# Kernel optimization log

Measured on AMD Instinct MI355X. Metric: run time of the kernel, lower is better.

## Reference

```python
import jax, jax.numpy as jnp
import numpy as np

H, D, K, FF = 4, 256, 1024, 1024  # n_head, d_model, key_feature_dim, dim_feedforward
L, B = 2048, 4                    # pixels, batch


def setup_inputs() -> dict:
    key = jax.random.key(0)
    ks = jax.random.split(key, 12)
    def g(k, shape, s=0.02):
        return jax.random.normal(k, shape, jnp.float32) * s
    return dict(
        src=jax.random.normal(ks[0], (L, B, D), jnp.float32),
        WK=g(ks[1], (H, K, D), (2.0 / K) ** 0.5),
        WQ=g(ks[2], (H, K, D), (2.0 / K) ** 0.5),
        WV=g(ks[3], (H, D, D), (2.0 / D) ** 0.5),
        TC=g(ks[4], (H, D, D)),
        ENw1=g(ks[5], (H, FF, D)), ENb1=jnp.zeros((H, FF), jnp.float32),
        ENw2=g(ks[6], (H, D, FF)), ENb2=jnp.zeros((H, D), jnp.float32),
        ENg=jnp.ones((H, D), jnp.float32), ENbeta=jnp.zeros((H, D), jnp.float32),
        Wout=g(ks[7], (D, H * D)),
        L1w=g(ks[8], (FF, D)), L1b=jnp.zeros((FF,), jnp.float32),
        L2w=g(ks[9], (D, FF)), L2b=jnp.zeros((D,), jnp.float32),
        N1g=jnp.ones((D,), jnp.float32), N1b=jnp.zeros((D,), jnp.float32),
        N2g=jnp.ones((D,), jnp.float32), N2b=jnp.zeros((D,), jnp.float32),
    )


def _ln(x, g, b, eps=1e-5):
    m = jnp.mean(x, -1, keepdims=True)
    v = jnp.mean((x - m) ** 2, -1, keepdims=True)
    return (x - m) * jax.lax.rsqrt(v + eps) * g + b


def _l2n(x, eps=1e-12):
    n = jnp.sqrt(jnp.sum(x * x, -1, keepdims=True))
    return x / jnp.maximum(n, eps)


def reference(src, WK, WQ, WV, TC, ENw1, ENb1, ENw2, ENb2, ENg, ENbeta,
              Wout, L1w, L1b, L2w, L2b, N1g, N1b, N2g, N2b):
    # --- RMA: per-head RelationUnit, vectorized over head axis h ---
    wq = _l2n(jnp.einsum('lbd,hkd->hlbk', src, WQ))   # (H,L,B,K), L2-normed
    wk = _l2n(jnp.einsum('lbd,hkd->hlbk', src, WK))
    wv = jnp.einsum('lbd,hed->hlbe', src, WV)         # (H,L,B,D)
    dot = jnp.einsum('hlbk,hmbk->hblm', wq, wk)       # (H,B,Lq,Lk)
    aff = jax.nn.softmax(dot, axis=-1)                 # softmax over keys (temp=1)
    aff = aff / (1e-9 + jnp.sum(aff, axis=2, keepdims=True))  # renorm over QUERY dim (torch dim=1)
    out = jnp.einsum('hblm,hmbe->hlbe', aff, wv)       # (H,L,B,D)
    ru = jax.nn.relu(jnp.einsum('hlbe,hfe->hlbf', src[None] - out, TC))
    # per-head extra TransNonlinear: residual MLP + layernorm
    hid = jax.nn.relu(jnp.einsum('hlbd,hfd->hlbf', ru, ENw1) + ENb1[:, None, None, :])
    s2 = jnp.einsum('hlbf,hdf->hlbd', hid, ENw2) + ENb2[:, None, None, :]
    tn = _ln(ru + s2, ENg[:, None, None, :], ENbeta[:, None, None, :])  # (H,L,B,D)
    concat = jnp.transpose(tn, (1, 2, 0, 3)).reshape(L, B, H * D)
    attn = concat @ Wout.T                              # (L,B,D)
    # --- encoder layer: residual + LN + FFN + LN (dropout = eval identity) ---
    x = _ln(src + attn, N1g, N1b)
    ff = jax.nn.relu(x @ L1w.T + L1b) @ L2w.T + L2b
    return _ln(x + ff, N2g, N2b)
```

## Files before the change

### kernel.cpp

```cpp
#include <hip/hip_runtime.h>
#include <hip/hip_bf16.h>

typedef __hip_bfloat16 bf16;
typedef short s16x8 __attribute__((ext_vector_type(8)));
typedef float f32x4 __attribute__((ext_vector_type(4)));

#define HN 4
#define DM 256
#define KF 1024
#define FFD 1024
#define LL 2048
#define BB 4
#define NN (LL * BB)
#define HD (HN * DM)

__device__ __forceinline__ float b2f(unsigned short u) {
    unsigned v = ((unsigned)u) << 16; float f; __builtin_memcpy(&f, &v, 4); return f;
}
__device__ __forceinline__ unsigned short f2b(float f) {
    bf16 b = (bf16)f; unsigned short u; __builtin_memcpy(&u, &b, 2); return u;
}

__device__ __forceinline__ float waveReduceSum(float v) {
    for (int o = 32; o; o >>= 1) v += __shfl_down(v, o, 64);
    return v;
}
__device__ __forceinline__ float waveReduceMax(float v) {
    for (int o = 32; o; o >>= 1) v = fmaxf(v, __shfl_down(v, o, 64));
    return v;
}
__device__ __forceinline__ float blockReduceSum(float v) {
    __shared__ float sh[4];
    v = waveReduceSum(v);
    __syncthreads();
    if ((threadIdx.x & 63) == 0) sh[threadIdx.x >> 6] = v;
    __syncthreads();
    return sh[0] + sh[1] + sh[2] + sh[3];
}
__device__ __forceinline__ float blockReduceMax(float v) {
    __shared__ float sh[4];
    v = waveReduceMax(v);
    __syncthreads();
    if ((threadIdx.x & 63) == 0) sh[threadIdx.x >> 6] = v;
    __syncthreads();
    return fmaxf(fmaxf(sh[0], sh[1]), fmaxf(sh[2], sh[3]));
}

__global__ void sentinel_kernel(float* out, float val) {
    if (threadIdx.x == 0 && blockIdx.x == 0) out[0] = val;
}

__device__ __forceinline__ void gll16(const void* g, void* l) {
#if defined(__HIP_DEVICE_COMPILE__)
    __builtin_amdgcn_global_load_lds(
        (const __attribute__((address_space(1))) unsigned int*)g,
        (__attribute__((address_space(3))) unsigned int*)l, 16, 0, 0);
#endif
}

#define VMC(n) asm volatile("s_waitcnt vmcnt(" #n ")" ::: "memory")
#define LGKM0() asm volatile("s_waitcnt lgkmcnt(0)" ::: "memory")

__global__ __launch_bounds__(512) void gemm256(
    const bf16* __restrict__ A, int lda, long sA,
    const bf16* __restrict__ Bv, int ldb, long sB,
    void* __restrict__ C, int cF32, int ldc, long sC,
    int Kc,
    const float* __restrict__ bias, long sBias,
    const void* __restrict__ aux, int auxType, int ldaux, long sAux,
    float accSign, int relu)
{
    const int z = blockIdx.z;
    const bf16* Ah = A + (long)z * sA;
    const bf16* Bh = Bv + (long)z * sB;
    float* Cf = (float*)C + (long)z * sC;
    bf16*  Ch = (bf16*)C + (long)z * sC;
    const float* biasp = bias ? (bias + (long)z * sBias) : nullptr;
    const float* auxf = (auxType == 1) ? ((const float*)aux + (long)z * sAux) : nullptr;
    const bf16*  auxh = (auxType == 2) ? ((const bf16*)aux + (long)z * sAux) : nullptr;

    __shared__ __align__(16) bf16 As[2][256 * 64];
    __shared__ __align__(16) bf16 Bs[2][256 * 64];

    const int tid  = threadIdx.x;
    const int lane = tid & 63;
    const int wid  = __builtin_amdgcn_readfirstlane(tid >> 6);
    const int wm   = wid >> 2;
    const int wn   = wid & 3;
    const int lrow = lane & 15;
    const int quad = lane >> 4;
    const int m0 = blockIdx.x * 256;
    const int n0 = blockIdx.y * 256;

    const int srow8  = wid * 8 + (lane >> 3);
    const int scolsw = ((lane & 7) * 8) ^ ((srow8 & 7) << 3);
    const bf16* Aorg = Ah + (long)m0 * lda;
    const bf16* Borg = Bh + (long)n0 * ldb;

    const int colx = (lane & 7) << 3;
    const int kc0 = (quad * 8) ^ colx;
    const int kc1 = (32 + quad * 8) ^ colx;

    f32x4 acc[8][4] = {};
    s16x8 afr[4][2], bfr[4][2];

    const int nk = Kc >> 6;

    auto stg = [&](const bf16* org, int ld, bf16* lds, int k0, int h) {
#pragma unroll
        for (int j = 0; j < 2; j++) {
            int rl = h * 128 + j * 64 + srow8;
            gll16((const void*)(org + (long)rl * ld + k0 + scolsw),
                  (void*)(lds + (h * 128 + j * 64 + wid * 8) * 64));
        }
    };

    stg(Aorg, lda, As[0], 0, 0); stg(Aorg, lda, As[0], 0, 1);
    stg(Borg, ldb, Bs[0], 0, 0); stg(Borg, ldb, Bs[0], 0, 1);
    if (nk > 1) {
        stg(Aorg, lda, As[1], 64, 0); stg(Aorg, lda, As[1], 64, 1);
        stg(Borg, ldb, Bs[1], 64, 0); stg(Borg, ldb, Bs[1], 64, 1);
        VMC(8);
    } else {
        VMC(0);
    }
    __builtin_amdgcn_s_barrier();

    for (int t = 0; t < nk; ++t) {
        const int s = t & 1;
        const bf16* Acur = As[s];
        const bf16* Bcur = Bs[s];
        bf16* Anxt = As[s ^ 1];
        bf16* Bslot = Bs[s];
        const bool stA = (t >= 1) && (t + 1 < nk);
        const bool stB = (t + 2 < nk);

#pragma unroll
        for (int mi = 0; mi < 4; mi++) {
            int r = (wm * 128 + mi * 16 + lrow) * 64;
            afr[mi][0] = *(const s16x8*)&Acur[r + kc0];
            afr[mi][1] = *(const s16x8*)&Acur[r + kc1];
        }
#pragma unroll
        for (int ni = 0; ni < 2; ni++) {
            int r = (wn * 64 + ni * 16 + lrow) * 64;
            bfr[ni][0] = *(const s16x8*)&Bcur[r + kc0];
            bfr[ni][1] = *(const s16x8*)&Bcur[r + kc1];
        }
        if (stA) stg(Aorg, lda, Anxt, (t + 1) << 6, 0);
        __builtin_amdgcn_s_barrier();
        LGKM0();
        __builtin_amdgcn_s_setprio(1);
#pragma unroll
        for (int mi = 0; mi < 4; mi++)
#pragma unroll
            for (int ni = 0; ni < 2; ni++)
#pragma unroll
                for (int ks = 0; ks < 2; ks++)
                    acc[mi][ni] = __builtin_amdgcn_mfma_f32_16x16x32_bf16(afr[mi][ks], bfr[ni][ks], acc[mi][ni], 0, 0, 0);
        __builtin_amdgcn_s_setprio(0);
        __builtin_amdgcn_s_barrier();

#pragma unroll
        for (int ni = 0; ni < 2; ni++) {
            int r = (wn * 64 + (2 + ni) * 16 + lrow) * 64;
            bfr[2 + ni][0] = *(const s16x8*)&Bcur[r + kc0];
            bfr[2 + ni][1] = *(const s16x8*)&Bcur[r + kc1];
        }
        if (stA) stg(Aorg, lda, Anxt, (t + 1) << 6, 1);
        __builtin_amdgcn_s_barrier();
        LGKM0();
        __builtin_amdgcn_s_setprio(1);
#pragma unroll
        for (int mi = 0; mi < 4; mi++)
#pragma unroll
            for (int ni = 0; ni < 2; ni++)
#pragma unroll
                for (int ks = 0; ks < 2; ks++)
                    acc[mi][2 + ni] = __builtin_amdgcn_mfma_f32_16x16x32_bf16(afr[mi][ks], bfr[2 + ni][ks], acc[mi][2 + ni], 0, 0, 0);
        __builtin_amdgcn_s_setprio(0);
        __builtin_amdgcn_s_barrier();

#pragma unroll
        for (int mi = 0; mi < 4; mi++) {
            int r = (wm * 128 + 64 + mi * 16 + lrow) * 64;
            afr[mi][0] = *(const s16x8*)&Acur[r + kc0];
            afr[mi][1] = *(const s16x8*)&Acur[r + kc1];
        }
        if (stB) stg(Borg, ldb, Bslot, (t + 2) << 6, 0);
        __builtin_amdgcn_s_barrier();
        LGKM0();
        __builtin_amdgcn_s_setprio(1);
#pragma unroll
        for (int mi = 0; mi < 4; mi++)
#pragma unroll
            for (int ni = 0; ni < 2; ni++)
#pragma unroll
                for (int ks = 0; ks < 2; ks++)
                    acc[4 + mi][ni] = __builtin_amdgcn_mfma_f32_16x16x32_bf16(afr[mi][ks], bfr[ni][ks], acc[4 + mi][ni], 0, 0, 0);
        __builtin_amdgcn_s_setprio(0);
        __builtin_amdgcn_s_barrier();

        if (stB) stg(Borg, ldb, Bslot, (t + 2) << 6, 1);
        __builtin_amdgcn_s_barrier();
        __builtin_amdgcn_s_setprio(1);
#pragma unroll
        for (int mi = 0; mi < 4; mi++)
#pragma unroll
            for (int ni = 0; ni < 2; ni++)
#pragma unroll
                for (int ks = 0; ks < 2; ks++)
                    acc[4 + mi][2 + ni] = __builtin_amdgcn_mfma_f32_16x16x32_bf16(afr[mi][ks], bfr[2 + ni][ks], acc[4 + mi][2 + ni], 0, 0, 0);
        __builtin_amdgcn_s_setprio(0);
        if (stB) { VMC(4); } else { VMC(0); }
        __builtin_amdgcn_s_barrier();
    }

#pragma unroll
    for (int mi = 0; mi < 8; mi++) {
#pragma unroll
        for (int ni = 0; ni < 4; ni++) {
            int col = n0 + wn * 64 + ni * 16 + lrow;
            float bvl = biasp ? biasp[col] : 0.0f;
#pragma unroll
            for (int i = 0; i < 4; i++) {
                int row = m0 + wm * 128 + mi * 16 + quad * 4 + i;
                float v = accSign * acc[mi][ni][i] + bvl;
                if (auxType == 1) v += auxf[(long)row * ldaux + col];
                else if (auxType == 2) v += (float)auxh[(long)row * ldaux + col];
                if (relu) v = fmaxf(v, 0.0f);
                if (cF32) Cf[(long)row * ldc + col] = v;
                else Ch[(long)row * ldc + col] = (bf16)v;
            }
        }
    }
}

template<int BN>
__global__ __launch_bounds__(256) void gemm_nt(
    const void* __restrict__ A, int aF32, int lda, long sA,
    const void* __restrict__ Bv, int bF32, int ldb, long sB,
    void* __restrict__ C, int cF32, int ldc, long sC,
    int Kc,
    const float* __restrict__ bias, long sBias,
    const void* __restrict__ aux, int auxType, int ldaux, long sAux,
    float accSign, int relu)
{
    constexpr int NI = BN / 32;
    constexpr int WN = BN / 2;
    const int z = blockIdx.z;
    const float* Af = (const float*)A + (long)z * sA;
    const bf16*  Ah = (const bf16*)A + (long)z * sA;
    const float* Bf = (const float*)Bv + (long)z * sB;
    const bf16*  Bh = (const bf16*)Bv + (long)z * sB;
    float* Cf = (float*)C + (long)z * sC;
    bf16*  Ch = (bf16*)C + (long)z * sC;
    const float* biasp = bias ? (bias + (long)z * sBias) : nullptr;
    const float* auxf = (auxType == 1) ? ((const float*)aux + (long)z * sAux) : nullptr;
    const bf16*  auxh = (auxType == 2) ? ((const bf16*)aux + (long)z * sAux) : nullptr;

    __shared__ __align__(16) bf16 As[3][128 * 32];
    __shared__ __align__(16) bf16 Bs[3][BN * 32];

    const int tid = threadIdx.x;
    const int lane = tid & 63;
    const int wv = __builtin_amdgcn_readfirstlane(tid >> 6);
    const int wm = (tid >> 6) & 1;
    const int wn = (tid >> 6) >> 1;
    const int lrow = lane & 15;
    const int quad = lane >> 4;
    const int m0 = blockIdx.x * 128;
    const int n0 = blockIdx.y * BN;
    const int srow = tid >> 1;
    const int scol = (tid & 1) * 16;
    const int drow = wv * 16 + (lane >> 2);
    const int dcol = (lane & 3) * 8;

    f32x4 acc[4][NI] = {};

    if (!aF32 && !bF32) {
        const int nk = Kc >> 5;
        auto stage = [&](int t) {
            const int buf = t % 3;
            const int k0 = t << 5;
            const bf16* a0 = Ah + (long)(m0 + drow) * lda + k0 + dcol;
            gll16((const void*)a0, (void*)&As[buf][wv * 512]);
            gll16((const void*)(a0 + (long)lda * 64), (void*)&As[buf][2048 + wv * 512]);
            const bf16* b0 = Bh + (long)(n0 + drow) * ldb + k0 + dcol;
            gll16((const void*)b0, (void*)&Bs[buf][wv * 512]);
            if (BN == 128)
                gll16((const void*)(b0 + (long)ldb * 64), (void*)&Bs[buf][2048 + wv * 512]);
        };
        stage(0);
        if (nk > 1) {
            stage(1);
            if constexpr (BN == 128) { VMC(4); } else { VMC(3); }
        } else {
            VMC(0);
        }
        __builtin_amdgcn_s_barrier();
        for (int t = 0; t < nk; ++t) {
            const int cur = t % 3;
            if (t + 2 < nk) stage(t + 2);
            s16x8 af[4], bfg[NI];
#pragma unroll
            for (int mi = 0; mi < 4; mi++)
                af[mi] = *(const s16x8*)&As[cur][(wm * 64 + mi * 16 + lrow) * 32 + quad * 8];
#pragma unroll
            for (int ni = 0; ni < NI; ni++)
                bfg[ni] = *(const s16x8*)&Bs[cur][(wn * WN + ni * 16 + lrow) * 32 + quad * 8];
#pragma unroll
            for (int mi = 0; mi < 4; mi++)
#pragma unroll
                for (int ni = 0; ni < NI; ni++)
                    acc[mi][ni] = __builtin_amdgcn_mfma_f32_16x16x32_bf16(af[mi], bfg[ni], acc[mi][ni], 0, 0, 0);
            if (t + 2 < nk) {
                if constexpr (BN == 128) { VMC(4); } else { VMC(3); }
            } else {
                VMC(0);
            }
            __builtin_amdgcn_s_barrier();
        }
    } else {
        for (int k0 = 0; k0 < Kc; k0 += 32) {
            uint4 av0, av1, bv0, bv1;
            if (aF32) {
                const float* ag = Af + (long)(m0 + srow) * lda + k0 + scol;
                ushort t[16];
#pragma unroll
                for (int j = 0; j < 4; j++) {
                    float4 f = *(const float4*)(ag + 4 * j);
                    t[4*j] = f2b(f.x); t[4*j+1] = f2b(f.y); t[4*j+2] = f2b(f.z); t[4*j+3] = f2b(f.w);
                }
                av0 = *(const uint4*)&t[0]; av1 = *(const uint4*)&t[8];
            }
            if (bF32) {
                if (srow < BN) {
                    const float* bg = Bf + (long)(n0 + srow) * ldb + k0 + scol;
                    ushort t[16];
#pragma unroll
                    for (int j = 0; j < 4; j++) {
                        float4 f = *(const float4*)(bg + 4 * j);
                        t[4*j] = f2b(f.x); t[4*j+1] = f2b(f.y); t[4*j+2] = f2b(f.z); t[4*j+3] = f2b(f.w);
                    }
                    bv0 = *(const uint4*)&t[0]; bv1 = *(const uint4*)&t[8];
                }
            }
            __syncthreads();
            if (aF32) {
                *(uint4*)&As[0][srow * 32 + scol] = av0;
                *(uint4*)&As[0][srow * 32 + scol + 8] = av1;
            } else {
                gll16((const void*)(Ah + (long)(m0 + drow) * lda + k0 + dcol), (void*)&As[0][wv * 512]);
                gll16((const void*)(Ah + (long)(m0 + 64 + drow) * lda + k0 + dcol), (void*)&As[0][2048 + wv * 512]);
            }
            if (bF32) {
                if (srow < BN) {
                    *(uint4*)&Bs[0][srow * 32 + scol] = bv0;
                    *(uint4*)&Bs[0][srow * 32 + scol + 8] = bv1;
                }
            } else {
                gll16((const void*)(Bh + (long)(n0 + drow) * ldb + k0 + dcol), (void*)&Bs[0][wv * 512]);
                if (BN == 128)
                    gll16((const void*)(Bh + (long)(n0 + 64 + drow) * ldb + k0 + dcol), (void*)&Bs[0][2048 + wv * 512]);
            }
            __syncthreads();

            s16x8 af[4], bfg[NI];
#pragma unroll
            for (int mi = 0; mi < 4; mi++)
                af[mi] = *(const s16x8*)&As[0][(wm * 64 + mi * 16 + lrow) * 32 + quad * 8];
#pragma unroll
            for (int ni = 0; ni < NI; ni++)
                bfg[ni] = *(const s16x8*)&Bs[0][(wn * WN + ni * 16 + lrow) * 32 + quad * 8];
#pragma unroll
            for (int mi = 0; mi < 4; mi++)
#pragma unroll
                for (int ni = 0; ni < NI; ni++)
                    acc[mi][ni] = __builtin_amdgcn_mfma_f32_16x16x32_bf16(af[mi], bfg[ni], acc[mi][ni], 0, 0, 0);
        }
    }

#pragma unroll
    for (int mi = 0; mi < 4; mi++) {
#pragma unroll
        for (int ni = 0; ni < NI; ni++) {
            int col = n0 + wn * WN + ni * 16 + lrow;
            float bvl = biasp ? biasp[col] : 0.0f;
#pragma unroll
            for (int i = 0; i < 4; i++) {
                int row = m0 + wm * 64 + mi * 16 + quad * 4 + i;
                float v = accSign * acc[mi][ni][i] + bvl;
                if (auxType == 1) v += auxf[(long)row * ldaux + col];
                else if (auxType == 2) v += (float)auxh[(long)row * ldaux + col];
                if (relu) v = fmaxf(v, 0.0f);
                if (cF32) Cf[(long)row * ldc + col] = v;
                else Ch[(long)row * ldc + col] = (bf16)v;
            }
        }
    }
}

__global__ __launch_bounds__(256) void cvt4(const float* __restrict__ in, bf16* __restrict__ out, int n4) {
    int i = blockIdx.x * 256 + threadIdx.x;
    if (i < n4) {
        float4 f = ((const float4*)in)[i];
        ushort4 u; u.x = f2b(f.x); u.y = f2b(f.y); u.z = f2b(f.z); u.w = f2b(f.w);
        ((ushort4*)out)[i] = u;
    }
}

struct WCvt {
    const float* in[16];
    bf16* out[16];
    int n4[16];
};
__global__ __launch_bounds__(256) void cvt_weights(WCvt wc) {
    int t = blockIdx.y;
    int n4 = wc.n4[t];
    const float4* in = (const float4*)wc.in[t];
    ushort4* out = (ushort4*)wc.out[t];
    for (int i = blockIdx.x * 256 + threadIdx.x; i < n4; i += gridDim.x * 256) {
        float4 f = in[i];
        ushort4 u; u.x = f2b(f.x); u.y = f2b(f.y); u.z = f2b(f.z); u.w = f2b(f.w);
        out[i] = u;
    }
}

__global__ __launch_bounds__(256) void l2norm_rows(bf16* __restrict__ Q) {
    bf16* q = Q + (long)blockIdx.x * KF;
    ushort4 u = ((ushort4*)q)[threadIdx.x];
    float v0 = b2f(u.x), v1 = b2f(u.y), v2 = b2f(u.z), v3 = b2f(u.w);
    float ss = blockReduceSum(v0 * v0 + v1 * v1 + v2 * v2 + v3 * v3);
    float inv = 1.0f / fmaxf(sqrtf(ss), 1e-12f);
    u.x = f2b(v0 * inv); u.y = f2b(v1 * inv); u.z = f2b(v2 * inv); u.w = f2b(v3 * inv);
    ((ushort4*)q)[threadIdx.x] = u;
}

__global__ __launch_bounds__(256) void l2norm2(bf16* __restrict__ QK) {
    bf16* q = QK + (long)blockIdx.x * 2048 + (long)blockIdx.y * 1024;
    ushort4 u = ((ushort4*)q)[threadIdx.x];
    float v0 = b2f(u.x), v1 = b2f(u.y), v2 = b2f(u.z), v3 = b2f(u.w);
    float ss = blockReduceSum(v0 * v0 + v1 * v1 + v2 * v2 + v3 * v3);
    float inv = 1.0f / fmaxf(sqrtf(ss), 1e-12f);
    u.x = f2b(v0 * inv); u.y = f2b(v1 * inv); u.z = f2b(v2 * inv); u.w = f2b(v3 * inv);
    ((ushort4*)q)[threadIdx.x] = u;
}

__global__ __launch_bounds__(256) void softmax_rows(bf16* __restrict__ P) {
    bf16* p = P + (long)blockIdx.x * LL;
    ushort4 a = ((ushort4*)p)[2 * threadIdx.x];
    ushort4 b = ((ushort4*)p)[2 * threadIdx.x + 1];
    float v[8] = {b2f(a.x), b2f(a.y), b2f(a.z), b2f(a.w), b2f(b.x), b2f(b.y), b2f(b.z), b2f(b.w)};
    float mx = -1e30f;
#pragma unroll
    for (int i = 0; i < 8; i++) mx = fmaxf(mx, v[i]);
    mx = blockReduceMax(mx);
    float s = 0.0f;
#pragma unroll
    for (int i = 0; i < 8; i++) { v[i] = __expf(v[i] - mx); s += v[i]; }
    s = blockReduceSum(s);
    float inv = 1.0f / s;
    a.x = f2b(v[0]*inv); a.y = f2b(v[1]*inv); a.z = f2b(v[2]*inv); a.w = f2b(v[3]*inv);
    b.x = f2b(v[4]*inv); b.y = f2b(v[5]*inv); b.z = f2b(v[6]*inv); b.w = f2b(v[7]*inv);
    ((ushort4*)p)[2 * threadIdx.x] = a;
    ((ushort4*)p)[2 * threadIdx.x + 1] = b;
}

__global__ __launch_bounds__(256) void zero_cs(float* __restrict__ cs) {
    cs[blockIdx.x * 256 + threadIdx.x] = 0.0f;
}

__global__ __launch_bounds__(256) void colsum2(const bf16* __restrict__ P, float* __restrict__ cs) {
    int col = blockIdx.x * 256 + threadIdx.x;
    int rc = blockIdx.y;
    int b = blockIdx.z;
    const bf16* p = P + (long)b * LL * LL + (long)rc * 128 * LL + col;
    float s = 0.0f;
#pragma unroll 4
    for (int r = 0; r < 128; r++) s += (float)p[(long)r * LL];
    atomicAdd(&cs[(long)b * LL + col], s);
}

__global__ __launch_bounds__(256) void scale_vt(bf16* __restrict__ vt, const float* __restrict__ cs) {
    int e = blockIdx.x, b = blockIdx.y;
    bf16* row = vt + ((long)b * DM + e) * LL;
    const float* c = cs + (long)b * LL;
#pragma unroll
    for (int i = 0; i < 8; i++) {
        int m = threadIdx.x + i * 256;
        row[m] = (bf16)((float)row[m] / (1e-9f + c[m]));
    }
}

__global__ __launch_bounds__(256) void ln_rows(const bf16* __restrict__ in, void* __restrict__ out,
                                               int outF32,
                                               const float* __restrict__ g, const float* __restrict__ b,
                                               const float* __restrict__ aux) {
    long base = (long)blockIdx.x * 256;
    float v = (float)in[base + threadIdx.x];
    if (aux) v += aux[base + threadIdx.x];
    float mean = blockReduceSum(v) * (1.0f / 256.0f);
    float d = v - mean;
    float var = blockReduceSum(d * d) * (1.0f / 256.0f);
    float o = d * rsqrtf(var + 1e-5f) * g[threadIdx.x] + b[threadIdx.x];
    if (outF32) ((float*)out)[base + threadIdx.x] = o;
    else ((bf16*)out)[base + threadIdx.x] = (bf16)o;
}

__global__ __launch_bounds__(256) void ln_cat(bf16* __restrict__ cat, const float* __restrict__ g,
                                              const float* __restrict__ bb) {
    long n = blockIdx.x;
    int h = blockIdx.y;
    bf16* x = cat + n * HD + (long)h * DM;
    float v = (float)x[threadIdx.x];
    float mean = blockReduceSum(v) * (1.0f / 256.0f);
    float d = v - mean;
    float var = blockReduceSum(d * d) * (1.0f / 256.0f);
    x[threadIdx.x] = (bf16)(d * rsqrtf(var + 1e-5f) * g[h * DM + threadIdx.x] + bb[h * DM + threadIdx.x]);
}

extern "C" void kernel_launch(void* const* d_in, const int* in_sizes, int n_in,
                              void* d_out, int out_size, void* d_ws, size_t ws_size,
                              hipStream_t stream) {
    const float* src  = (const float*)d_in[0];
    const float* WK   = (const float*)d_in[1];
    const float* WQ   = (const float*)d_in[2];
    const float* WV   = (const float*)d_in[3];
    const float* TC   = (const float*)d_in[4];
    const float* ENw1 = (const float*)d_in[5];
    const float* ENb1 = (const float*)d_in[6];
    const float* ENw2 = (const float*)d_in[7];
    const float* ENb2 = (const float*)d_in[8];
    const float* ENg  = (const float*)d_in[9];
    const float* ENbt = (const float*)d_in[10];
    const float* Wout = (const float*)d_in[11];
    const float* L1w  = (const float*)d_in[12];
    const float* L1b  = (const float*)d_in[13];
    const float* L2w  = (const float*)d_in[14];
    const float* L2b  = (const float*)d_in[15];
    const float* N1g  = (const float*)d_in[16];
    const float* N1b  = (const float*)d_in[17];
    const float* N2g  = (const float*)d_in[18];
    const float* N2b  = (const float*)d_in[19];

    const size_t COMPACT_FLOOR = 34700000;
    const size_t FAST_FLOOR  = 92307456;
    const size_t FASTW_FLOOR = 92307456 + 11010048;
    if (ws_size < COMPACT_FLOOR || out_size != NN * DM || n_in != 20) {
        float val;
        if (n_in != 20) val = 32768.0f + (float)n_in;
        else if (out_size != NN * DM) val = 49152.0f;
        else val = 16384.0f + 128.0f * (float)(unsigned)(ws_size >> 20);
        sentinel_kernel<<<1, 64, 0, stream>>>((float*)d_out, val);
        return;
    }

    char* w = (char*)d_ws;
    auto G = [&](const void* A, int aF, int lda, long sA,
                 const void* B, int bF, int ldb, long sB,
                 void* C, int cF, int ldc, long sC,
                 int M, int Nn, int Kc, int nb,
                 const float* bias, long sBias,
                 const void* aux, int auxT, int ldaux, long sAux,
                 float sgn, int relu) {
        gemm_nt<128><<<dim3(M / 128, Nn / 128, nb), dim3(256), 0, stream>>>(
            A, aF, lda, sA, B, bF, ldb, sB, C, cF, ldc, sC, Kc,
            bias, sBias, aux, auxT, ldaux, sAux, sgn, relu);
    };
    auto G64 = [&](const void* A, int aF, int lda, long sA,
                 const void* B, int bF, int ldb, long sB,
                 void* C, int cF, int ldc, long sC,
                 int M, int Nn, int Kc, int nb,
                 const float* bias, long sBias,
                 const void* aux, int auxT, int ldaux, long sAux,
                 float sgn, int relu) {
        gemm_nt<64><<<dim3(M / 128, Nn / 64, nb), dim3(256), 0, stream>>>(
            A, aF, lda, sA, B, bF, ldb, sB, C, cF, ldc, sC, Kc,
            bias, sBias, aux, auxT, ldaux, sAux, sgn, relu);
    };
    auto G2 = [&](const void* A, int lda, long sA,
                  const void* B, int ldb, long sB,
                  void* C, int cF, int ldc, long sC,
                  int M, int Nn, int Kc, int nb,
                  const float* bias, long sBias,
                  const void* aux, int auxT, int ldaux, long sAux,
                  float sgn, int relu) {
        gemm256<<<dim3(M / 256, Nn / 256, nb), dim3(512), 0, stream>>>(
            (const bf16*)A, lda, sA, (const bf16*)B, ldb, sB, C, cF, ldc, sC, Kc,
            bias, sBias, aux, auxT, ldaux, sAux, sgn, relu);
    };

    if (ws_size >= FAST_FLOOR) {
        bf16*  Sb  = (bf16*)(w + 0);
        bf16*  Q   = (bf16*)(w + 4194304);
        bf16*  K   = (bf16*)(w + 20971520);
        bf16*  Vt  = (bf16*)(w + 37748736);
        bf16*  P   = (bf16*)(w + 41943040);
        bf16*  Su  = (bf16*)(w + 75497472);
        float* Cs  = (float*)(w + 92274688);
        bf16* QK = Q;
        bf16* Ru = Q; bf16* Hid = K; bf16* Cat = P;
        bf16* Attn = Vt; bf16* Xln = Su; bf16* Ffh = Q; bf16* Yp = Vt;

        const int haveWb = (ws_size >= FASTW_FLOOR) ? 1 : 0;
        char* wb = w + 92307456;
        bf16* WQKb  = (bf16*)(wb + 0);
        bf16* WVb   = (bf16*)(wb + 4194304);
        bf16* TCb   = (bf16*)(wb + 4718592);
        bf16* ENw1b = (bf16*)(wb + 5242880);
        bf16* ENw2b = (bf16*)(wb + 7340032);
        bf16* Woutb = (bf16*)(wb + 9437184);
        bf16* L1wb  = (bf16*)(wb + 9961472);
        bf16* L2wb  = (bf16*)(wb + 10485760);
        if (haveWb) {
            WCvt wc;
            for (int h = 0; h < HN; h++) {
                wc.in[2*h]   = WQ + (long)h * KF * DM; wc.out[2*h]   = WQKb + (long)h * 2048 * DM;            wc.n4[2*h]   = 65536;
                wc.in[2*h+1] = WK + (long)h * KF * DM; wc.out[2*h+1] = WQKb + (long)h * 2048 * DM + KF * DM;  wc.n4[2*h+1] = 65536;
            }
            wc.in[8]  = WV;   wc.out[8]  = WVb;   wc.n4[8]  = 65536;
            wc.in[9]  = TC;   wc.out[9]  = TCb;   wc.n4[9]  = 65536;
            wc.in[10] = ENw1; wc.out[10] = ENw1b; wc.n4[10] = 262144;
            wc.in[11] = ENw2; wc.out[11] = ENw2b; wc.n4[11] = 262144;
            wc.in[12] = Wout; wc.out[12] = Woutb; wc.n4[12] = 65536;
            wc.in[13] = L1w;  wc.out[13] = L1wb;  wc.n4[13] = 65536;
            wc.in[14] = L2w;  wc.out[14] = L2wb;  wc.n4[14] = 65536;
            cvt_weights<<<dim3(256, 15), 256, 0, stream>>>(wc);
        }
        const int wF = haveWb ? 0 : 1;
        auto WP = [&](const void* f32p, const void* b16p, long off) {
            return haveWb ? (const void*)((const bf16*)b16p + off)
                          : (const void*)((const float*)f32p + off);
        };

        cvt4<<<2048, 256, 0, stream>>>(src, Sb, NN * DM / 4);

        for (int h = 0; h < HN; h++) {
            if (haveWb) {
                G2(Sb, DM, 0, WQKb + (long)h * 2048 * DM, DM, 0, QK, 0, 2048, 0,
                   NN, 2048, DM, 1, nullptr, 0, nullptr, 0, 0, 0, 1.0f, 0);
            } else {
                G(Sb, 0, DM, 0, WQ + (long)h * KF * DM, 1, DM, 0, QK, 0, 2048, 0,
                  NN, KF, DM, 1, nullptr, 0, nullptr, 0, 0, 0, 1.0f, 0);
                G(Sb, 0, DM, 0, WK + (long)h * KF * DM, 1, DM, 0, QK + KF, 0, 2048, 0,
                  NN, KF, DM, 1, nullptr, 0, nullptr, 0, 0, 0, 1.0f, 0);
            }
            G64(WP(WV, WVb, (long)h * DM * DM), wF, DM, 0, Sb, 0, BB * DM, DM,
              Vt, 0, LL, (long)DM * LL,
              DM, LL, DM, BB, nullptr, 0, nullptr, 0, 0, 0, 1.0f, 0);
            l2norm2<<<dim3(NN, 2), 256, 0, stream>>>(QK);
            G2(QK, 4 * 2048, 2048, QK + 1024, 4 * 2048, 2048, P, 0, LL, (long)LL * LL,
               LL, LL, KF, BB, nullptr, 0, nullptr, 0, 0, 0, 1.0f, 0);
            softmax_rows<<<BB * LL, 256, 0, stream>>>(P);
            zero_cs<<<BB * LL / 256, 256, 0, stream>>>(Cs);
            colsum2<<<dim3(LL / 256, 16, BB), 256, 0, stream>>>(P, Cs);
            scale_vt<<<dim3(DM, BB), 256, 0, stream>>>(Vt, Cs);
            G64(P, 0, LL, (long)LL * LL, Vt, 0, LL, (long)DM * LL,
              Su + (long)h * NN * DM, 0, BB * DM, DM,
              LL, DM, LL, BB, nullptr, 0, Sb, 2, BB * DM, DM, -1.0f, 0);
        }
        G(Su, 0, DM, (long)NN * DM, WP(TC, TCb, 0), wF, DM, (long)DM * DM,
          Ru, 0, DM, (long)NN * DM,
          NN, DM, DM, HN, nullptr, 0, nullptr, 0, 0, 0, 1.0f, 1);
        for (int h = 0; h < HN; h++) {
            G(Ru + (long)h * NN * DM, 0, DM, 0, WP(ENw1, ENw1b, (long)h * FFD * DM), wF, DM, 0,
              Hid, 0, FFD, 0, NN, FFD, DM, 1, ENb1 + (long)h * FFD, 0, nullptr, 0, 0, 0, 1.0f, 1);
            G64(Hid, 0, FFD, 0, WP(ENw2, ENw2b, (long)h * DM * FFD), wF, FFD, 0,
              Cat + (long)h * DM, 0, HD, 0, NN, DM, FFD, 1,
              ENb2 + (long)h * DM, 0, Ru + (long)h * NN * DM, 2, DM, 0, 1.0f, 0);
        }
        ln_cat<<<dim3(NN, HN), 256, 0, stream>>>(Cat, ENg, ENbt);
        G64(Cat, 0, HD, 0, WP(Wout, Woutb, 0), wF, HD, 0, Attn, 0, DM, 0,
          NN, DM, HD, 1, nullptr, 0, nullptr, 0, 0, 0, 1.0f, 0);
        ln_rows<<<NN, 256, 0, stream>>>(Attn, Xln, 0, N1g, N1b, src);
        G(Xln, 0, DM, 0, WP(L1w, L1wb, 0), wF, DM, 0, Ffh, 0, FFD, 0,
          NN, FFD, DM, 1, L1b, 0, nullptr, 0, 0, 0, 1.0f, 1);
        G64(Ffh, 0, FFD, 0, WP(L2w, L2wb, 0), wF, FFD, 0, Yp, 0, DM, 0,
          NN, DM, FFD, 1, L2b, 0, Xln, 2, DM, 0, 1.0f, 0);
        ln_rows<<<NN, 256, 0, stream>>>(Yp, (float*)d_out, 1, N2g, N2b, nullptr);
    } else {
        bf16*  S0 = (bf16*)(w + 0);
        bf16*  S1 = (bf16*)(w + 16777216);
        bf16*  S2 = (bf16*)(w + 20971520);
        bf16*  S3 = (bf16*)(w + 25165824);
        bf16*  S4 = (bf16*)(w + 26214400);
        bf16*  S5 = (bf16*)(w + 30408704);
        float* Cs = (float*)(w + 34603008);

        for (int h = 0; h < HN; h++) {
            for (int b = 0; b < BB; b++) {
                G(src + b * DM, 1, BB * DM, 0, WQ + (long)h * KF * DM, 1, DM, 0,
                  S1, 0, KF, 0, LL, KF, DM, 1, nullptr, 0, nullptr, 0, 0, 0, 1.0f, 0);
                G(src + b * DM, 1, BB * DM, 0, WK + (long)h * KF * DM, 1, DM, 0,
                  S2, 0, KF, 0, LL, KF, DM, 1, nullptr, 0, nullptr, 0, 0, 0, 1.0f, 0);
                G(WV + (long)h * DM * DM, 1, DM, 0, src + b * DM, 1, BB * DM, 0,
                  S3, 0, LL, 0, DM, LL, DM, 1, nullptr, 0, nullptr, 0, 0, 0, 1.0f, 0);
                l2norm_rows<<<LL, 256, 0, stream>>>(S1);
                l2norm_rows<<<LL, 256, 0, stream>>>(S2);
                G(S1, 0, KF, 0, S2, 0, KF, 0, S0, 0, LL, 0,
                  LL, LL, KF, 1, nullptr, 0, nullptr, 0, 0, 0, 1.0f, 0);
                softmax_rows<<<LL, 256, 0, stream>>>(S0);
                zero_cs<<<LL / 256, 256, 0, stream>>>(Cs);
                colsum2<<<dim3(LL / 256, 16, 1), 256, 0, stream>>>(S0, Cs);
                scale_vt<<<dim3(DM, 1), 256, 0, stream>>>(S3, Cs);
                G(S0, 0, LL, 0, S3, 0, LL, 0, S4 + b * DM, 0, BB * DM, 0,
                  LL, DM, LL, 1, nullptr, 0, src + b * DM, 1, BB * DM, 0, -1.0f, 0);
            }
            G(S4, 0, DM, 0, TC + (long)h * DM * DM, 1, DM, 0, S1, 0, DM, 0,
              NN, DM, DM, 1, nullptr, 0, nullptr, 0, 0, 0, 1.0f, 1);
            G(S1, 0, DM, 0, ENw1 + (long)h * FFD * DM, 1, DM, 0, S0, 0, FFD, 0,
              NN, FFD, DM, 1, ENb1 + (long)h * FFD, 0, nullptr, 0, 0, 0, 1.0f, 1);
            G(S0, 0, FFD, 0, ENw2 + (long)h * DM * FFD, 1, FFD, 0, S2, 0, DM, 0,
              NN, DM, FFD, 1, ENb2 + (long)h * DM, 0, S1, 2, DM, 0, 1.0f, 0);
            ln_rows<<<NN, 256, 0, stream>>>(S2, S2, 0, ENg + (long)h * DM, ENbt + (long)h * DM, nullptr);
            G(S2, 0, DM, 0, Wout + (long)h * DM, 1, HD, 0, S5, 0, DM, 0,
              NN, DM, DM, 1, nullptr, 0, (h == 0) ? nullptr : (const void*)S5,
              (h == 0) ? 0 : 2, DM, 0, 1.0f, 0);
        }
        ln_rows<<<NN, 256, 0, stream>>>(S5, S1, 0, N1g, N1b, src);
        G(S1, 0, DM, 0, L1w, 1, DM, 0, S0, 0, FFD, 0,
          NN, FFD, DM, 1, L1b, 0, nullptr, 0, 0, 0, 1.0f, 1);
        G(S0, 0, FFD, 0, L2w, 1, FFD, 0, S2, 0, DM, 0,
          NN, DM, FFD, 1, L2b, 0, S1, 2, DM, 0, 1.0f, 0);
        ln_rows<<<NN, 256, 0, stream>>>(S2, (float*)d_out, 1, N2g, N2b, nullptr);
    }
}
```

Before: 1.061 ms.

## Swizzle GEMM tile order across XCDs and split Q/K into separate buffers

Remaps GEMM block indices so that consecutive tiles are grouped onto the same XCD, aiming for better L2 reuse of shared A/B panels on MI355X. It also stores Q and K projections as separate contiguous buffers (batched GEMM over two outputs) instead of one interleaved 2048-wide buffer. The QK^T GEMM then reads rows with a stride of 4096 instead of 8192. The l2norm kernel indexing is updated to match. The swizzle adds a little index arithmetic per block and only applies when the grid size is a multiple of 8.

Result: no change. 1.076 ms (+1.5%).

```diff
diff --git a/kernel.cpp b/kernel.cpp
--- a/kernel.cpp
+++ b/kernel.cpp
@@ -60,6 +60,17 @@
 
 #define VMC(n) asm volatile("s_waitcnt vmcnt(" #n ")" ::: "memory")
 #define LGKM0() asm volatile("s_waitcnt lgkmcnt(0)" ::: "memory")
+
+__device__ __forceinline__ void xcd_swz(int& bx, int& by) {
+    int gx = gridDim.x;
+    int n2 = gx * gridDim.y;
+    if ((n2 & 7) == 0) {
+        int f = bx + by * gx;
+        int fs = (f & 7) * (n2 >> 3) + (f >> 3);
+        bx = fs % gx;
+        by = fs / gx;
+    }
+}
 
 __global__ __launch_bounds__(512) void gemm256(
     const bf16* __restrict__ A, int lda, long sA,
@@ -89,8 +100,10 @@
     const int wn   = wid & 3;
     const int lrow = lane & 15;
     const int quad = lane >> 4;
-    const int m0 = blockIdx.x * 256;
-    const int n0 = blockIdx.y * 256;
+    int bx = blockIdx.x, by = blockIdx.y;
+    xcd_swz(bx, by);
+    const int m0 = bx * 256;
+    const int n0 = by * 256;
 
     const int srow8  = wid * 8 + (lane >> 3);
     const int scolsw = ((lane & 7) * 8) ^ ((srow8 & 7) << 3);
@@ -269,8 +282,10 @@
     const int wn = (tid >> 6) >> 1;
     const int lrow = lane & 15;
     const int quad = lane >> 4;
-    const int m0 = blockIdx.x * 128;
-    const int n0 = blockIdx.y * BN;
+    int bx = blockIdx.x, by = blockIdx.y;
+    xcd_swz(bx, by);
+    const int m0 = bx * 128;
+    const int n0 = by * BN;
     const int srow = tid >> 1;
     const int scol = (tid & 1) * 16;
     const int drow = wv * 16 + (lane >> 2);
@@ -438,7 +453,7 @@
 }
 
 __global__ __launch_bounds__(256) void l2norm2(bf16* __restrict__ QK) {
-    bf16* q = QK + (long)blockIdx.x * 2048 + (long)blockIdx.y * 1024;
+    bf16* q = QK + (long)blockIdx.y * ((long)NN * KF) + (long)blockIdx.x * KF;
     ushort4 u = ((ushort4*)q)[threadIdx.x];
     float v0 = b2f(u.x), v1 = b2f(u.y), v2 = b2f(u.z), v3 = b2f(u.w);
     float ss = blockReduceSum(v0 * v0 + v1 * v1 + v2 * v2 + v3 * v3);
@@ -599,7 +614,6 @@
         bf16*  P   = (bf16*)(w + 41943040);
         bf16*  Su  = (bf16*)(w + 75497472);
         float* Cs  = (float*)(w + 92274688);
-        bf16* QK = Q;
         bf16* Ru = Q; bf16* Hid = K; bf16* Cat = P;
         bf16* Attn = Vt; bf16* Xln = Su; bf16* Ffh = Q; bf16* Yp = Vt;
 
@@ -638,19 +652,20 @@
 
         for (int h = 0; h < HN; h++) {
             if (haveWb) {
-                G2(Sb, DM, 0, WQKb + (long)h * 2048 * DM, DM, 0, QK, 0, 2048, 0,
-                   NN, 2048, DM, 1, nullptr, 0, nullptr, 0, 0, 0, 1.0f, 0);
+                G2(Sb, DM, 0, WQKb + (long)h * 2048 * DM, DM, (long)KF * DM,
+                   Q, 0, KF, (long)NN * KF,
+                   NN, KF, DM, 2, nullptr, 0, nullptr, 0, 0, 0, 1.0f, 0);
             } else {
-                G(Sb, 0, DM, 0, WQ + (long)h * KF * DM, 1, DM, 0, QK, 0, 2048, 0,
+                G(Sb, 0, DM, 0, WQ + (long)h * KF * DM, 1, DM, 0, Q, 0, KF, 0,
                   NN, KF, DM, 1, nullptr, 0, nullptr, 0, 0, 0, 1.0f, 0);
-                G(Sb, 0, DM, 0, WK + (long)h * KF * DM, 1, DM, 0, QK + KF, 0, 2048, 0,
+                G(Sb, 0, DM, 0, WK + (long)h * KF * DM, 1, DM, 0, K, 0, KF, 0,
                   NN, KF, DM, 1, nullptr, 0, nullptr, 0, 0, 0, 1.0f, 0);
             }
             G64(WP(WV, WVb, (long)h * DM * DM), wF, DM, 0, Sb, 0, BB * DM, DM,
               Vt, 0, LL, (long)DM * LL,
               DM, LL, DM, BB, nullptr, 0, nullptr, 0, 0, 0, 1.0f, 0);
-            l2norm2<<<dim3(NN, 2), 256, 0, stream>>>(QK);
-            G2(QK, 4 * 2048, 2048, QK + 1024, 4 * 2048, 2048, P, 0, LL, (long)LL * LL,
+            l2norm2<<<dim3(NN, 2), 256, 0, stream>>>(Q);
+            G2(Q, BB * KF, KF, K, BB * KF, KF, P, 0, LL, (long)LL * LL,
                LL, LL, KF, BB, nullptr, 0, nullptr, 0, 0, 0, 1.0f, 0);
             softmax_rows<<<BB * LL, 256, 0, stream>>>(P);
             zero_cs<<<BB * LL / 256, 256, 0, stream>>>(Cs);
```
